# Performance work log

Measured on AMD Instinct MI355X. Metric: run time of the kernel, lower is better.

## Reference

```python
import jax, jax.numpy as jnp
import numpy as np

NUM_NODES = 2_000_000
NUM_PINS = 8_000_000


def setup_inputs() -> dict:
    key = jax.random.key(0)
    k1, k2, k3 = jax.random.split(key, 3)
    # CSR offsets: sorted, pinned to [0, NUM_PINS]
    starts = jnp.sort(jax.random.randint(k1, (NUM_NODES + 1,), 0, NUM_PINS + 1, dtype=jnp.int32))
    starts = starts.at[0].set(0).at[-1].set(NUM_PINS)
    # flat node->pin map: a permutation of all pin ids (each pin belongs to one node)
    flat_node2pin = jax.random.permutation(k2, NUM_PINS).astype(jnp.int32)
    # per-pin sort key (a permutation -> unique keys, like a global pin ordering)
    sorted_pin_map = jax.random.permutation(k3, NUM_PINS).astype(jnp.int32)
    return {
        "flat_node2pin_start": starts,
        "flat_node2pin": flat_node2pin,
        "sorted_pin_map": sorted_pin_map,
        "num_nodes": NUM_NODES,
    }


def reference(flat_node2pin_start, flat_node2pin, sorted_pin_map, num_nodes):
    """For each node, return the pin id (from its CSR segment) with the minimum
    sorted_pin_map value; 0 for nodes with no pins (matching zeros init)."""
    num_pins = flat_node2pin.shape[0]
    pin_pos = jnp.arange(num_pins, dtype=jnp.int32)
    # segment id for each flat pin slot: node i owns [starts[i], starts[i+1])
    seg = (jnp.searchsorted(flat_node2pin_start, pin_pos, side="right") - 1).astype(jnp.int32)
    key = sorted_pin_map[flat_node2pin]  # ordering key per flat slot
    min_key = jax.ops.segment_min(key, seg, num_segments=num_nodes)  # [num_nodes]
    # pick the pin achieving the min key (ties -> smallest pin id, keys unique here)
    cand = jnp.where(key == min_key[seg], flat_node2pin, jnp.int32(num_pins))
    best_pin = jax.ops.segment_min(cand, seg, num_segments=num_nodes)
    counts = flat_node2pin_start[1:] - flat_node2pin_start[:-1]
    node2pinId = jnp.where(counts > 0, best_pin, jnp.int32(0)).astype(jnp.int32)
    return node2pinId
```

## Files before the change

### kernel.cpp

```cpp
#include <hip/hip_runtime.h>
#include <stdint.h>


typedef int iv4 __attribute__((ext_vector_type(4)));

#define NPB 256
#define CAP 3072

__global__ void build_key4_kernel(const int* __restrict__ key,
                                  uint32_t* __restrict__ key4,
                                  int num_pins, int shift) {
    int t = blockIdx.x * blockDim.x + threadIdx.x;
    int base = t * 8;
    if (base >= num_pins) return;
    if (base + 8 <= num_pins) {
        const iv4* kp = (const iv4*)(key + base);
        iv4 a = __builtin_nontemporal_load(kp);
        iv4 b = __builtin_nontemporal_load(kp + 1);
        uint32_t w = 0;
        w |= (((uint32_t)a.x >> shift) & 15u) << 0;
        w |= (((uint32_t)a.y >> shift) & 15u) << 4;
        w |= (((uint32_t)a.z >> shift) & 15u) << 8;
        w |= (((uint32_t)a.w >> shift) & 15u) << 12;
        w |= (((uint32_t)b.x >> shift) & 15u) << 16;
        w |= (((uint32_t)b.y >> shift) & 15u) << 20;
        w |= (((uint32_t)b.z >> shift) & 15u) << 24;
        w |= (((uint32_t)b.w >> shift) & 15u) << 28;
        __builtin_nontemporal_store(w, key4 + t);
    } else {
        uint32_t w = 0;
        for (int j = 0; base + j < num_pins; ++j) {
            uint32_t k = (uint32_t)key[base + j];
            w |= ((k >> shift) & 15u) << (4 * j);
        }
        __builtin_nontemporal_store(w, key4 + t);
    }
}

__device__ __forceinline__ uint32_t nib_of(const uint32_t* key4, uint32_t p) {
    uint32_t w = key4[p >> 3];
    return (w >> ((p & 7u) * 4u)) & 15u;
}

__global__ __launch_bounds__(256) void SortNode2Pin_stage_kernel(
        const int* __restrict__ starts,
        const int* __restrict__ n2p,
        const int* __restrict__ key,
        const uint32_t* __restrict__ key4,
        int* __restrict__ out,
        int num_nodes) {
    __shared__ int B[NPB + 1];
    __shared__ uint32_t slot[CAP + 4];

    int t = threadIdx.x;
    int i0 = blockIdx.x * NPB;

    {
        int idx = i0 + t; if (idx > num_nodes) idx = num_nodes;
        B[t] = starts[idx];
        if (t == 0) {
            int idx2 = i0 + NPB; if (idx2 > num_nodes) idx2 = num_nodes;
            B[NPB] = starts[idx2];
        }
    }
    __syncthreads();

    int jbeg0 = B[0];
    int jend0 = B[NPB];
    int range = jend0 - jbeg0;

    if (range <= CAP) {
        int jal = jbeg0 & ~3;
        int nch = (jend0 - jal + 3) >> 2;
        for (int c = t; c < nch; c += NPB) {
            int j0 = jal + (c << 2);
            uint32_t sv0, sv1, sv2, sv3;
            if (j0 >= jbeg0 && j0 + 4 <= jend0) {
                iv4 p4 = __builtin_nontemporal_load((const iv4*)(n2p + j0));
                uint32_t p0 = (uint32_t)p4.x, p1 = (uint32_t)p4.y;
                uint32_t p2 = (uint32_t)p4.z, p3 = (uint32_t)p4.w;
                sv0 = (nib_of(key4, p0) << 23) | p0;
                sv1 = (nib_of(key4, p1) << 23) | p1;
                sv2 = (nib_of(key4, p2) << 23) | p2;
                sv3 = (nib_of(key4, p3) << 23) | p3;
            } else {
                uint32_t sv[4];
                #pragma unroll
                for (int e = 0; e < 4; ++e) {
                    int j = j0 + e;
                    if (j >= jbeg0 && j < jend0) {
                        uint32_t p = (uint32_t)__builtin_nontemporal_load(n2p + j);
                        sv[e] = (nib_of(key4, p) << 23) | p;
                    } else {
                        sv[e] = 0xFFFFFFFFu;
                    }
                }
                sv0 = sv[0]; sv1 = sv[1]; sv2 = sv[2]; sv3 = sv[3];
            }
            iv4 w4; w4.x = (int)sv0; w4.y = (int)sv1; w4.z = (int)sv2; w4.w = (int)sv3;
            *(iv4*)&slot[c << 2] = w4;
        }
        __syncthreads();

        int s = B[t] - jal;
        int e = B[t + 1] - jal;
        int mv = 16, cnt = 0;
        uint32_t bp = 0;
        for (int q = s; q < e; ++q) {
            uint32_t sp = slot[q];
            int nib = (int)(sp >> 23);
            if (nib < mv) { mv = nib; cnt = 1; bp = sp & 0x7FFFFFu; }
            else if (nib == mv) ++cnt;
        }
        int r = (int)bp;
        if (cnt > 1) {
            int bk = 0x7fffffff;
            for (int q = s; q < e; ++q) {
                uint32_t sp = slot[q];
                if ((int)(sp >> 23) == mv) {
                    int p = (int)(sp & 0x7FFFFFu);
                    int k = key[p];
                    if (k < bk) { bk = k; r = p; }
                }
            }
        }
        int node = i0 + t;
        if (node < num_nodes) __builtin_nontemporal_store(r, out + node);
    } else {
        int node = i0 + t;
        if (node < num_nodes) {
            int s = B[t], e = B[t + 1];
            int mv = 16, bp = 0, bk = -1;
            for (int j = s; j < e; ++j) {
                uint32_t p = (uint32_t)n2p[j];
                int n = (int)nib_of(key4, p);
                if (n > mv) continue;
                if (n < mv) { mv = n; bp = (int)p; bk = -1; }
                else {
                    if (bk < 0) bk = key[bp];
                    int k = key[p];
                    if (k < bk) { bk = k; bp = (int)p; }
                }
            }
            __builtin_nontemporal_store(bp, out + node);
        }
    }
}

__global__ void SortNode2Pin_direct_kernel(const int* __restrict__ starts,
                                           const int* __restrict__ n2p,
                                           const int* __restrict__ key,
                                           int* __restrict__ out,
                                           int num_nodes) {
    int i = blockIdx.x * blockDim.x + threadIdx.x;
    if (i >= num_nodes) return;
    int s = starts[i];
    int e = starts[i + 1];
    int best_pin = 0;
    int best_key = 0x7fffffff;
    for (int j = s; j < e; ++j) {
        int p = n2p[j];
        int k = key[p];
        if (k < best_key) { best_key = k; best_pin = p; }
    }
    out[i] = best_pin;
}

extern "C" void kernel_launch(void* const* d_in, const int* in_sizes, int n_in,
                              void* d_out, int out_size, void* d_ws, size_t ws_size,
                              hipStream_t stream) {
    const int* starts = (const int*)d_in[0];
    const int* n2p    = (const int*)d_in[1];
    const int* key    = (const int*)d_in[2];
    int num_nodes = out_size;
    int num_pins  = in_sizes[1];

    size_t key4_words = (size_t)((num_pins + 7) / 8);
    size_t need = key4_words * sizeof(uint32_t);

    int block = 256;
    if (ws_size >= need && num_pins < (1 << 23)) {
        int bits = 32 - __builtin_clz((unsigned)(num_pins - 1));
        int shift = bits > 4 ? bits - 4 : 0;
        uint32_t* key4 = (uint32_t*)d_ws;

        int g1 = (int)((key4_words + block - 1) / block);
        build_key4_kernel<<<g1, block, 0, stream>>>(key, key4, num_pins, shift);

        int g2 = (num_nodes + NPB - 1) / NPB;
        SortNode2Pin_stage_kernel<<<g2, block, 0, stream>>>(
            starts, n2p, key, key4, (int*)d_out, num_nodes);
    } else {
        int grid = (num_nodes + block - 1) / block;
        SortNode2Pin_direct_kernel<<<grid, block, 0, stream>>>(
            starts, n2p, key, (int*)d_out, num_nodes);
    }
}
```

Measured before the change: 93.72 us.

## Process two nodes per thread with unrolled staging and vectorized LDS scan

```diff
diff --git a/kernel.cpp b/kernel.cpp
--- a/kernel.cpp
+++ b/kernel.cpp
@@ -4,8 +4,9 @@
 
 typedef int iv4 __attribute__((ext_vector_type(4)));
 
-#define NPB 256
-#define CAP 3072
+#define NPB 512
+#define NT  256
+#define CAP 2560
 
 __global__ void build_key4_kernel(const int* __restrict__ key,
                                   uint32_t* __restrict__ key4,
@@ -42,7 +43,62 @@
     return (w >> ((p & 7u) * 4u)) & 15u;
 }
 
-__global__ __launch_bounds__(256) void SortNode2Pin_stage_kernel(
+__device__ __forceinline__ iv4 load_chunk(const int* __restrict__ n2p,
+                                          int jal, int jbeg, int jend, int c) {
+    int j0 = jal + (c << 2);
+    if (j0 >= jbeg && j0 + 4 <= jend) {
+        return __builtin_nontemporal_load((const iv4*)(n2p + j0));
+    }
+    iv4 r;
+    #pragma unroll
+    for (int e = 0; e < 4; ++e) {
+        int j = j0 + e;
+        r[e] = (j >= jbeg && j < jend) ? __builtin_nontemporal_load(n2p + j)
+                                       : -1;
+    }
+    return r;
+}
+
+__device__ __forceinline__ uint32_t pack_sv(const uint32_t* key4, int pi) {
+    if (pi < 0) return 0xFFFFFFFFu;
+    uint32_t p = (uint32_t)pi;
+    return (nib_of(key4, p) << 23) | p;
+}
+
+__device__ __forceinline__ int scan_seg(const uint32_t* slot, int s, int e,
+                                        const int* __restrict__ key) {
+    int mv = 1 << 30;
+    int cnt = 0;
+    uint32_t bp = 0;
+    for (int q = (s & ~3); q < e; q += 4) {
+        iv4 v = *(const iv4*)(slot + q);
+        #pragma unroll
+        for (int u = 0; u < 4; ++u) {
+            int j = q + u;
+            uint32_t sp = (uint32_t)v[u];
+            int nib = (int)(sp >> 23);
+            if (j >= s && j < e) {
+                if (nib < mv) { mv = nib; cnt = 1; bp = sp & 0x7FFFFFu; }
+                else if (nib == mv) ++cnt;
+            }
+        }
+    }
+    int r = (int)bp;
+    if (cnt > 1) {
+        int bk = 0x7fffffff;
+        for (int q = s; q < e; ++q) {
+            uint32_t sp = slot[q];
+            if ((int)(sp >> 23) == mv) {
+                int p = (int)(sp & 0x7FFFFFu);
+                int k = key[p];
+                if (k < bk) { bk = k; r = p; }
+            }
+        }
+    }
+    return r;
+}
+
+__global__ __launch_bounds__(NT) void SortNode2Pin_stage_kernel(
         const int* __restrict__ starts,
         const int* __restrict__ n2p,
         const int* __restrict__ key,
@@ -50,18 +106,14 @@
         int* __restrict__ out,
         int num_nodes) {
     __shared__ int B[NPB + 1];
-    __shared__ uint32_t slot[CAP + 4];
+    __shared__ __align__(16) uint32_t slot[CAP + 8];
 
     int t = threadIdx.x;
     int i0 = blockIdx.x * NPB;
 
-    {
-        int idx = i0 + t; if (idx > num_nodes) idx = num_nodes;
-        B[t] = starts[idx];
-        if (t == 0) {
-            int idx2 = i0 + NPB; if (idx2 > num_nodes) idx2 = num_nodes;
-            B[NPB] = starts[idx2];
-        }
+    for (int idx = t; idx <= NPB; idx += NT) {
+        int g = i0 + idx; if (g > num_nodes) g = num_nodes;
+        B[idx] = starts[g];
     }
     __syncthreads();
 
@@ -72,64 +124,39 @@
     if (range <= CAP) {
         int jal = jbeg0 & ~3;
         int nch = (jend0 - jal + 3) >> 2;
-        for (int c = t; c < nch; c += NPB) {
-            int j0 = jal + (c << 2);
-            uint32_t sv0, sv1, sv2, sv3;
-            if (j0 >= jbeg0 && j0 + 4 <= jend0) {
-                iv4 p4 = __builtin_nontemporal_load((const iv4*)(n2p + j0));
-                uint32_t p0 = (uint32_t)p4.x, p1 = (uint32_t)p4.y;
-                uint32_t p2 = (uint32_t)p4.z, p3 = (uint32_t)p4.w;
-                sv0 = (nib_of(key4, p0) << 23) | p0;
-                sv1 = (nib_of(key4, p1) << 23) | p1;
-                sv2 = (nib_of(key4, p2) << 23) | p2;
-                sv3 = (nib_of(key4, p3) << 23) | p3;
-            } else {
-                uint32_t sv[4];
-                #pragma unroll
-                for (int e = 0; e < 4; ++e) {
-                    int j = j0 + e;
-                    if (j >= jbeg0 && j < jend0) {
-                        uint32_t p = (uint32_t)__builtin_nontemporal_load(n2p + j);
-                        sv[e] = (nib_of(key4, p) << 23) | p;
-                    } else {
-                        sv[e] = 0xFFFFFFFFu;
-                    }
-                }
-                sv0 = sv[0]; sv1 = sv[1]; sv2 = sv[2]; sv3 = sv[3];
-            }
-            iv4 w4; w4.x = (int)sv0; w4.y = (int)sv1; w4.z = (int)sv2; w4.w = (int)sv3;
-            *(iv4*)&slot[c << 2] = w4;
+        int c = t;
+        for (; c + NT < nch; c += 2 * NT) {
+            int c2 = c + NT;
+            iv4 pa = load_chunk(n2p, jal, jbeg0, jend0, c);
+            iv4 pb = load_chunk(n2p, jal, jbeg0, jend0, c2);
+            iv4 wa, wb;
+            #pragma unroll
+            for (int u = 0; u < 4; ++u) wa[u] = (int)pack_sv(key4, pa[u]);
+            #pragma unroll
+            for (int u = 0; u < 4; ++u) wb[u] = (int)pack_sv(key4, pb[u]);
+            *(iv4*)&slot[c  << 2] = wa;
+            *(iv4*)&slot[c2 << 2] = wb;
+        }
+        for (; c < nch; c += NT) {
+            iv4 pa = load_chunk(n2p, jal, jbeg0, jend0, c);
+            iv4 wa;
+            #pragma unroll
+            for (int u = 0; u < 4; ++u) wa[u] = (int)pack_sv(key4, pa[u]);
+            *(iv4*)&slot[c << 2] = wa;
         }
         __syncthreads();
 
-        int s = B[t] - jal;
-        int e = B[t + 1] - jal;
-        int mv = 16, cnt = 0;
-        uint32_t bp = 0;
-        for (int q = s; q < e; ++q) {
-            uint32_t sp = slot[q];
-            int nib = (int)(sp >> 23);
-            if (nib < mv) { mv = nib; cnt = 1; bp = sp & 0x7FFFFFu; }
-            else if (nib == mv) ++cnt;
-        }
-        int r = (int)bp;
-        if (cnt > 1) {
-            int bk = 0x7fffffff;
-            for (int q = s; q < e; ++q) {
-                uint32_t sp = slot[q];
-                if ((int)(sp >> 23) == mv) {
-                    int p = (int)(sp & 0x7FFFFFu);
-                    int k = key[p];
-                    if (k < bk) { bk = k; r = p; }
-                }
-            }
-        }
-        int node = i0 + t;
-        if (node < num_nodes) __builtin_nontemporal_store(r, out + node);
+        int ra = scan_seg(slot, B[t] - jal, B[t + 1] - jal, key);
+        int rb = scan_seg(slot, B[t + NT] - jal, B[t + NT + 1] - jal, key);
+        int na = i0 + t;
+        int nb = i0 + t + NT;
+        if (na < num_nodes) __builtin_nontemporal_store(ra, out + na);
+        if (nb < num_nodes) __builtin_nontemporal_store(rb, out + nb);
     } else {
-        int node = i0 + t;
-        if (node < num_nodes) {
-            int s = B[t], e = B[t + 1];
+        for (int idx = t; idx < NPB; idx += NT) {
+            int node = i0 + idx;
+            if (node >= num_nodes) break;
+            int s = B[idx], e = B[idx + 1];
             int mv = 16, bp = 0, bk = -1;
             for (int j = s; j < e; ++j) {
                 uint32_t p = (uint32_t)n2p[j];
@@ -178,21 +205,20 @@
     size_t key4_words = (size_t)((num_pins + 7) / 8);
     size_t need = key4_words * sizeof(uint32_t);
 
-    int block = 256;
     if (ws_size >= need && num_pins < (1 << 23)) {
         int bits = 32 - __builtin_clz((unsigned)(num_pins - 1));
         int shift = bits > 4 ? bits - 4 : 0;
         uint32_t* key4 = (uint32_t*)d_ws;
 
-        int g1 = (int)((key4_words + block - 1) / block);
-        build_key4_kernel<<<g1, block, 0, stream>>>(key, key4, num_pins, shift);
+        int g1 = (int)((key4_words + NT - 1) / NT);
+        build_key4_kernel<<<g1, NT, 0, stream>>>(key, key4, num_pins, shift);
 
         int g2 = (num_nodes + NPB - 1) / NPB;
-        SortNode2Pin_stage_kernel<<<g2, block, 0, stream>>>(
+        SortNode2Pin_stage_kernel<<<g2, NT, 0, stream>>>(
             starts, n2p, key, key4, (int*)d_out, num_nodes);
     } else {
-        int grid = (num_nodes + block - 1) / block;
-        SortNode2Pin_direct_kernel<<<grid, block, 0, stream>>>(
+        int grid = (num_nodes + 255) / 256;
+        SortNode2Pin_direct_kernel<<<grid, 256, 0, stream>>>(
             starts, n2p, key, (int*)d_out, num_nodes);
     }
 }
```

Result: faster. 91.10 us (-2.8%).
